# Kernel tuning notes

Hardware: AMD Instinct MI355X
Metric: run time of the kernel (lower is better)

Reference implementation:

```python
import jax, jax.numpy as jnp
import numpy as np

ARAP_WEIGHT = 1.0


def _decoder(code, W1, b1, W2, b2, W3, b3):
    # code: [D] -> vertices [N, 3]
    h = jax.nn.relu(code @ W1 + b1)
    h = jax.nn.relu(h @ W2 + b2)
    v = h @ W3 + b3
    return v.reshape(-1, 3)


def _arap_per_vertex(xyz1, recon, nbr, num_nbr, wmat):
    # xyz1, recon: [N,3]; nbr: [N,K] int; num_nbr: [N]; wmat: [N,K]
    N, K = nbr.shape
    mask = (jnp.arange(K)[None, :] < num_nbr[:, None]).astype(wmat.dtype)
    w = wmat * mask                              # zero out padded neighbors
    e_rest = xyz1[nbr] - xyz1[:, None, :]        # [N,K,3] rest-pose edges (gather)
    e_def = recon[nbr] - recon[:, None, :]       # [N,K,3] deformed edges (gather)
    # weighted covariance per vertex: S_i = sum_k w_ik e_ik e'_ik^T  -> [N,3,3]
    S = jnp.einsum('nk,nka,nkb->nab', w, e_rest, e_def)
    U, _, Vt = jnp.linalg.svd(S)
    V = jnp.swapaxes(Vt, -1, -2)
    R0 = jnp.einsum('nab,ncb->nac', V, U)        # V U^T
    d = jnp.linalg.det(R0)                       # reflection fix
    diag = jnp.stack([jnp.ones_like(d), jnp.ones_like(d), d], axis=-1)  # [N,3]
    R = jnp.einsum('nab,nb,ncb->nac', V, diag, U)
    R = jax.lax.stop_gradient(R)                 # local-global: rotations fixed in bwd
    e_rot = jnp.einsum('nab,nkb->nka', R, e_rest)
    resid = e_def - e_rot
    return jnp.sum(w * jnp.sum(resid * resid, axis=-1), axis=-1)  # [N]


def setup_inputs() -> dict:
    key = jax.random.key(0)
    ks = jax.random.split(key, 12)
    N, K, D = 20000, 16, 256
    H1, H2 = 512, 1024
    inp = {
        'code': jax.random.normal(ks[0], (D,), jnp.float32),
        'xyz1': jax.random.normal(ks[1], (N, 3), jnp.float32),
        'weightMatrix': jax.random.uniform(ks[2], (N, K), jnp.float32),
        'W1': jax.random.normal(ks[3], (D, H1), jnp.float32) * (1.0 / np.sqrt(D)),
        'b1': jax.random.normal(ks[4], (H1,), jnp.float32) * 0.01,
        'W2': jax.random.normal(ks[5], (H1, H2), jnp.float32) * (1.0 / np.sqrt(H1)),
        'b2': jax.random.normal(ks[6], (H2,), jnp.float32) * 0.01,
        'W3': jax.random.normal(ks[7], (H2, N * 3), jnp.float32) * (1.0 / np.sqrt(H2)),
        'b3': jax.random.normal(ks[8], (N * 3,), jnp.float32) * 0.01,
        'neighborsMatrix': jax.random.randint(ks[9], (N, K), 0, N, jnp.int64),
        'numNeighbors': jax.random.randint(ks[10], (N,), 0, 17, jnp.int64),
    }
    return inp


def reference(code, xyz1, weightMatrix, W1, b1, W2, b2, W3, b3,
              neighborsMatrix, numNeighbors):
    def energy(c):
        recon = _decoder(c, W1, b1, W2, b2, W3, b3)
        pv = _arap_per_vertex(xyz1, recon, neighborsMatrix, numNeighbors, weightMatrix)
        return ARAP_WEIGHT * jnp.mean(pv)

    E, g = jax.value_and_grad(energy)(code)
    # torch module returns (arapEnergy.item(), -code.grad) with arapEnergy = -E
    return (-E, g)
```

## Files before the change

### kernel.cpp

```cpp
#include <hip/hip_runtime.h>
#include <hip/hip_bf16.h>

#define N_V   20000
#define KNB   16
#define DCODE 256
#define H1    512
#define H2    1024
#define M3    60000

#define OFF_L2P   0
#define OFF_VPART 8192
#define OFF_V     488192
#define OFF_GV    548192
#define OFF_GZ2   608192
#define OFF_GZ1   609216
#define OFF_H1    609728
#define OFF_H2    610240
#define OFF_HC    611264
#define OFF_LIST  612288
#define OFF_CNT   613312
#define OFF_E     613316

__global__ void k_mlp12(const float* __restrict__ code, const float* __restrict__ W1,
                        const float* __restrict__ b1, const float* __restrict__ W2,
                        float* __restrict__ ws) {
    __shared__ float red[4][64];
    __shared__ float h1s[64];
    int t = threadIdx.x;
    int bx = blockIdx.x, dz = blockIdx.y;
    int d0 = dz * 64;

    int ln = t & 63, g = t >> 6;
    {
        float acc = 0.f;
        int r0 = g * 64;
#pragma unroll 8
        for (int rr = 0; rr < 64; ++rr)
            acc += code[r0 + rr] * W1[(size_t)(r0 + rr) * H1 + d0 + ln];
        red[g][ln] = acc;
    }
    __syncthreads();
    if (g == 0) {
        float h = fmaxf(red[0][ln] + red[1][ln] + red[2][ln] + red[3][ln] + b1[d0 + ln], 0.f);
        h1s[ln] = h;
        if (bx == 0) ws[OFF_H1 + d0 + ln] = h;
    }
    __syncthreads();

    int m = bx * 256 + t;
    float acc = 0.f;
#pragma unroll 8
    for (int dd = 0; dd < 64; ++dd)
        acc += h1s[dd] * W2[(size_t)(d0 + dd) * H2 + m];
    ws[OFF_L2P + dz * H2 + m] = acc;

    int gid = (dz * 4 + bx) * 256 + t;
    for (int idx = gid; idx < M3; idx += 8192) ws[OFF_GV + idx] = 0.f;
    if (gid == 0) { ws[OFF_E] = 0.f; ws[OFF_E + 1] = 0.f; }
}

__global__ void k_compact(const float* __restrict__ b2, float* __restrict__ ws) {
    __shared__ int scan[256];
    int t = threadIdx.x;
    float h[4]; int c = 0;
#pragma unroll
    for (int q = 0; q < 4; ++q) {
        int j = t * 4 + q;
        float s = b2[j];
#pragma unroll
        for (int p = 0; p < 8; ++p) s += ws[OFF_L2P + p * H2 + j];
        float hv = fmaxf(s, 0.f);
        ws[OFF_H2 + j] = hv;
        ws[OFF_GZ2 + j] = 0.f;
        h[q] = hv;
        c += (hv > 0.f) ? 1 : 0;
    }
    scan[t] = c;
    __syncthreads();
    for (int off = 1; off < 256; off <<= 1) {
        int x = (t >= off) ? scan[t - off] : 0;
        __syncthreads();
        scan[t] += x;
        __syncthreads();
    }
    int base = scan[t] - c;
    int* list = reinterpret_cast<int*>(&ws[OFF_LIST]);
#pragma unroll
    for (int q = 0; q < 4; ++q) {
        if (h[q] > 0.f) {
            list[base] = t * 4 + q;
            ws[OFF_HC + base] = h[q];
            ++base;
        }
    }
    if (t == 255) *reinterpret_cast<int*>(&ws[OFF_CNT]) = scan[255];
}

__global__ void k_l3p(const float* __restrict__ W3, float* __restrict__ ws) {
    __shared__ int   rlist[128];
    __shared__ float rh[128];
    int jz = blockIdx.y;
    int cnt = *reinterpret_cast<const int*>(&ws[OFF_CNT]);
    int per = (cnt + 7) >> 3;
    int s0 = jz * per;
    int s1 = s0 + per; if (s1 > cnt) s1 = cnt;
    int n = s1 - s0;
    int t = threadIdx.x;
    if (t < 128 && t < n) {
        rlist[t] = reinterpret_cast<const int*>(&ws[OFF_LIST])[s0 + t];
        rh[t]    = ws[OFF_HC + s0 + t];
    }
    __syncthreads();
    int m4 = blockIdx.x * 1024 + t * 4;
    if (m4 >= M3) return;
    float ax = 0.f, ay = 0.f, az = 0.f, aw = 0.f;
    int ii = 0;
    for (; ii + 7 < n; ii += 8) {
        float4 wv[8];
#pragma unroll
        for (int u = 0; u < 8; ++u)
            wv[u] = *reinterpret_cast<const float4*>(&W3[(size_t)rlist[ii + u] * M3 + m4]);
#pragma unroll
        for (int u = 0; u < 8; ++u) {
            float h = rh[ii + u];
            ax += h * wv[u].x; ay += h * wv[u].y; az += h * wv[u].z; aw += h * wv[u].w;
        }
    }
    for (; ii < n; ++ii) {
        float h = rh[ii];
        float4 wv = *reinterpret_cast<const float4*>(&W3[(size_t)rlist[ii] * M3 + m4]);
        ax += h * wv.x; ay += h * wv.y; az += h * wv.z; aw += h * wv.w;
    }
    *reinterpret_cast<float4*>(&ws[OFF_VPART + jz * M3 + m4]) =
        make_float4(ax, ay, az, aw);
}

__global__ void k_vred(const float* __restrict__ b3, float* __restrict__ ws) {
    int i4 = blockIdx.x * 256 + threadIdx.x;
    if (i4 < M3 / 4) {
        int m = i4 * 4;
        float4 a = *reinterpret_cast<const float4*>(&b3[m]);
#pragma unroll
        for (int jz = 0; jz < 8; ++jz) {
            float4 p = *reinterpret_cast<const float4*>(&ws[OFF_VPART + jz * M3 + m]);
            a.x += p.x; a.y += p.y; a.z += p.z; a.w += p.w;
        }
        *reinterpret_cast<float4*>(&ws[OFF_V + m]) = a;
    }
}


__device__ inline void jrotf(float a[3][3], float v[3][3], int p, int q) {
    float apq = a[p][q];
    if (fabsf(apq) < 1e-30f) return;
    float theta = (a[q][q] - a[p][p]) / (2.0f * apq);
    float t;
    if (fabsf(theta) > 1e18f) t = 0.5f / theta;
    else t = copysignf(1.0f, theta) / (fabsf(theta) + sqrtf(theta * theta + 1.0f));
    float c = 1.0f / sqrtf(t * t + 1.0f);
    float s = t * c;
    float app = a[p][p], aqq = a[q][q];
    a[p][p] = app - t * apq;
    a[q][q] = aqq + t * apq;
    a[p][q] = 0.0f; a[q][p] = 0.0f;
    int r = 3 - p - q;
    float arp = a[r][p], arq = a[r][q];
    a[r][p] = c * arp - s * arq; a[p][r] = a[r][p];
    a[r][q] = s * arp + c * arq; a[q][r] = a[r][q];
#pragma unroll
    for (int k2 = 0; k2 < 3; ++k2) {
        float vkp = v[k2][p], vkq = v[k2][q];
        v[k2][p] = c * vkp - s * vkq;
        v[k2][q] = s * vkp + c * vkq;
    }
}

__device__ void compute_Rf(const float S[3][3], float R[3][3]) {
    float A[3][3], V[3][3];
#pragma unroll
    for (int a = 0; a < 3; ++a)
#pragma unroll
        for (int b = 0; b < 3; ++b) {
            float s = 0.0f;
#pragma unroll
            for (int c = 0; c < 3; ++c) s += S[c][a] * S[c][b];
            A[a][b] = s;
            V[a][b] = (a == b) ? 1.0f : 0.0f;
        }
    for (int sweep = 0; sweep < 15; ++sweep) {
        float off = A[0][1]*A[0][1] + A[0][2]*A[0][2] + A[1][2]*A[1][2];
        float dg  = A[0][0]*A[0][0] + A[1][1]*A[1][1] + A[2][2]*A[2][2];
        if (off <= 1e-12f * (dg + 1e-30f)) break;
        jrotf(A, V, 0, 1); jrotf(A, V, 0, 2); jrotf(A, V, 1, 2);
    }
    int id[3] = {0, 1, 2};
    if (A[id[0]][id[0]] < A[id[1]][id[1]]) { int t = id[0]; id[0] = id[1]; id[1] = t; }
    if (A[id[0]][id[0]] < A[id[2]][id[2]]) { int t = id[0]; id[0] = id[2]; id[2] = t; }
    if (A[id[1]][id[1]] < A[id[2]][id[2]]) { int t = id[1]; id[1] = id[2]; id[2] = t; }
    float v0[3], v1[3], v2[3];
#pragma unroll
    for (int r = 0; r < 3; ++r) {
        v0[r] = V[r][id[0]]; v1[r] = V[r][id[1]]; v2[r] = V[r][id[2]];
    }
    float u0[3], u1[3], u2[3];
#pragma unroll
    for (int a = 0; a < 3; ++a)
        u0[a] = S[a][0]*v0[0] + S[a][1]*v0[1] + S[a][2]*v0[2];
    float n0 = sqrtf(u0[0]*u0[0] + u0[1]*u0[1] + u0[2]*u0[2]);
    if (!(n0 > 1e-20f)) {
#pragma unroll
        for (int a = 0; a < 3; ++a)
#pragma unroll
            for (int c = 0; c < 3; ++c) R[a][c] = (a == c) ? 1.0f : 0.0f;
        return;
    }
#pragma unroll
    for (int a = 0; a < 3; ++a) u0[a] /= n0;
    float t1[3];
#pragma unroll
    for (int a = 0; a < 3; ++a)
        t1[a] = S[a][0]*v1[0] + S[a][1]*v1[1] + S[a][2]*v1[2];
    float dp = u0[0]*t1[0] + u0[1]*t1[1] + u0[2]*t1[2];
#pragma unroll
    for (int a = 0; a < 3; ++a) t1[a] -= dp * u0[a];
    float n1 = sqrtf(t1[0]*t1[0] + t1[1]*t1[1] + t1[2]*t1[2]);
    if (n1 > 1e-5f * n0) {
#pragma unroll
        for (int a = 0; a < 3; ++a) u1[a] = t1[a] / n1;
    } else {
        int m = (fabsf(u0[0]) <= fabsf(u0[1]) && fabsf(u0[0]) <= fabsf(u0[2])) ? 0
              : (fabsf(u0[1]) <= fabsf(u0[2]) ? 1 : 2);
        float e[3] = {0.0f, 0.0f, 0.0f}; e[m] = 1.0f;
        float cx[3] = { u0[1]*e[2] - u0[2]*e[1],
                        u0[2]*e[0] - u0[0]*e[2],
                        u0[0]*e[1] - u0[1]*e[0] };
        float nn = sqrtf(cx[0]*cx[0] + cx[1]*cx[1] + cx[2]*cx[2]);
#pragma unroll
        for (int a = 0; a < 3; ++a) u1[a] = cx[a] / nn;
    }
    u2[0] = u0[1]*u1[2] - u0[2]*u1[1];
    u2[1] = u0[2]*u1[0] - u0[0]*u1[2];
    u2[2] = u0[0]*u1[1] - u0[1]*u1[0];
    float d = v0[0]*(v1[1]*v2[2] - v1[2]*v2[1])
            - v0[1]*(v1[0]*v2[2] - v1[2]*v2[0])
            + v0[2]*(v1[0]*v2[1] - v1[1]*v2[0]);
#pragma unroll
    for (int a = 0; a < 3; ++a)
#pragma unroll
        for (int c = 0; c < 3; ++c)
            R[a][c] = v0[a]*u0[c] + v1[a]*u1[c] + d * (v2[a]*u2[c]);
}

__global__ void k_arap(const float* __restrict__ xyz1, const float* __restrict__ wmat,
                       const int* __restrict__ nbr, const int* __restrict__ nnum,
                       float* __restrict__ ws) {
    const float* recon = ws + OFF_V;
    float* gv = ws + OFF_GV;
    int i = blockIdx.x * 256 + threadIdx.x;
    double pv = 0.0;
    if (i < N_V) {
        int num = nnum[i]; if (num > KNB) num = KNB;
        float cr0 = xyz1[3*i], cr1 = xyz1[3*i+1], cr2 = xyz1[3*i+2];
        float cd0 = recon[3*i], cd1 = recon[3*i+1], cd2 = recon[3*i+2];
        float er[KNB][3], ed[KNB][3], wk[KNB];
        int   jn[KNB];
        float S[3][3] = {{0,0,0},{0,0,0},{0,0,0}};
#pragma unroll
        for (int k = 0; k < KNB; ++k) {
            bool live = (k < num);
            int j = live ? nbr[i*KNB + k] : i;
            float w = live ? wmat[i*KNB + k] : 0.f;
            jn[k] = j; wk[k] = w;
            float e0 = xyz1[3*j]   - cr0, e1 = xyz1[3*j+1] - cr1, e2 = xyz1[3*j+2] - cr2;
            float f0 = recon[3*j]  - cd0, f1 = recon[3*j+1] - cd1, f2 = recon[3*j+2] - cd2;
            er[k][0] = e0; er[k][1] = e1; er[k][2] = e2;
            ed[k][0] = f0; ed[k][1] = f1; ed[k][2] = f2;
            S[0][0] += w*e0*f0; S[0][1] += w*e0*f1; S[0][2] += w*e0*f2;
            S[1][0] += w*e1*f0; S[1][1] += w*e1*f1; S[1][2] += w*e1*f2;
            S[2][0] += w*e2*f0; S[2][1] += w*e2*f1; S[2][2] += w*e2*f2;
        }
        float R[3][3];
        compute_Rf(S, R);
        const float gscale = 2.0f / (float)N_V;
        float own0 = 0.f, own1 = 0.f, own2 = 0.f;
#pragma unroll
        for (int k = 0; k < KNB; ++k) {
            if (k < num) {
                float w = wk[k];
                float r0 = ed[k][0] - (R[0][0]*er[k][0] + R[0][1]*er[k][1] + R[0][2]*er[k][2]);
                float r1 = ed[k][1] - (R[1][0]*er[k][0] + R[1][1]*er[k][1] + R[1][2]*er[k][2]);
                float r2 = ed[k][2] - (R[2][0]*er[k][0] + R[2][1]*er[k][1] + R[2][2]*er[k][2]);
                pv += (double)(w * (r0*r0 + r1*r1 + r2*r2));
                float g0 = gscale * w * r0;
                float g1 = gscale * w * r1;
                float g2 = gscale * w * r2;
                int j = jn[k];
                atomicAdd(&gv[3*j+0], g0);
                atomicAdd(&gv[3*j+1], g1);
                atomicAdd(&gv[3*j+2], g2);
                own0 += g0; own1 += g1; own2 += g2;
            }
        }
        if (num > 0) {
            atomicAdd(&gv[3*i+0], -own0);
            atomicAdd(&gv[3*i+1], -own1);
            atomicAdd(&gv[3*i+2], -own2);
        }
    }
#pragma unroll
    for (int m = 32; m; m >>= 1) pv += __shfl_xor(pv, m);
    __shared__ double wred[4];
    if ((threadIdx.x & 63) == 0) wred[threadIdx.x >> 6] = pv;
    __syncthreads();
    if (threadIdx.x == 0)
        atomicAdd(reinterpret_cast<double*>(ws + OFF_E),
                  wred[0] + wred[1] + wred[2] + wred[3]);
}


__global__ void k_gh2(const float* __restrict__ W3, float* __restrict__ ws) {
    int b = blockIdx.x;
    int cnt = *reinterpret_cast<const int*>(&ws[OFF_CNT]);
    if (2 * b >= cnt) return;
    const int* list = reinterpret_cast<const int*>(&ws[OFF_LIST]);
    int j0 = list[2 * b];
    bool has1 = (2 * b + 1 < cnt);
    int j1 = has1 ? list[2 * b + 1] : j0;
    const float4* w3r0 = reinterpret_cast<const float4*>(W3 + (size_t)j0 * M3);
    const float4* w3r1 = reinterpret_cast<const float4*>(W3 + (size_t)j1 * M3);
    const float4* gv4  = reinterpret_cast<const float4*>(ws + OFF_GV);
    float acc0 = 0.f, acc1 = 0.f;
    for (int it = threadIdx.x; it < M3 / 4; it += 256) {
        float4 g = gv4[it];
        float4 a = w3r0[it];
        float4 c = w3r1[it];
        acc0 += a.x*g.x + a.y*g.y + a.z*g.z + a.w*g.w;
        acc1 += c.x*g.x + c.y*g.y + c.z*g.z + c.w*g.w;
    }
    for (int m = 32; m; m >>= 1) {
        acc0 += __shfl_xor(acc0, m);
        acc1 += __shfl_xor(acc1, m);
    }
    __shared__ float wsum[4][2];
    if ((threadIdx.x & 63) == 0) {
        wsum[threadIdx.x >> 6][0] = acc0;
        wsum[threadIdx.x >> 6][1] = acc1;
    }
    __syncthreads();
    if (threadIdx.x == 0) {
        ws[OFF_GZ2 + j0] = wsum[0][0] + wsum[1][0] + wsum[2][0] + wsum[3][0];
        if (has1)
            ws[OFF_GZ2 + j1] = wsum[0][1] + wsum[1][1] + wsum[2][1] + wsum[3][1];
    }
}

__global__ void k_gh1(const float* __restrict__ W2, float* __restrict__ ws) {
    int wv = threadIdx.x >> 6, ln = threadIdx.x & 63;
    int i = blockIdx.x * 4 + wv;
    const float* gz2 = ws + OFF_GZ2;
    float acc = 0.f;
#pragma unroll
    for (int it = 0; it < H2 / 64; ++it) {
        int jj = ln + it * 64;
        acc += W2[(size_t)i * H2 + jj] * gz2[jj];
    }
    for (int m = 32; m; m >>= 1) acc += __shfl_xor(acc, m);
    if (ln == 0) ws[OFF_GZ1 + i] = (ws[OFF_H1 + i] > 0.f) ? acc : 0.f;
}

__global__ void k_gcode(const float* __restrict__ W1, float* __restrict__ ws,
                        float* __restrict__ out) {
    int wv = threadIdx.x >> 6, ln = threadIdx.x & 63;
    int d = blockIdx.x * 4 + wv;
    const float* gz1 = ws + OFF_GZ1;
    float acc = 0.f;
#pragma unroll
    for (int it = 0; it < H1 / 64; ++it) {
        int ii = ln + it * 64;
        acc += W1[(size_t)d * H1 + ii] * gz1[ii];
    }
    for (int m = 32; m; m >>= 1) acc += __shfl_xor(acc, m);
    if (ln == 0) out[1 + d] = acc;
    if (blockIdx.x == 0 && threadIdx.x == 0) {
        double E = *reinterpret_cast<const double*>(ws + OFF_E);
        out[0] = (float)(-(E / (double)N_V));
    }
}

extern "C" void kernel_launch(void* const* d_in, const int* in_sizes, int n_in,
                              void* d_out, int out_size, void* d_ws, size_t ws_size,
                              hipStream_t stream) {
    const float* code = (const float*)d_in[0];
    const float* xyz1 = (const float*)d_in[1];
    const float* wmat = (const float*)d_in[2];
    const float* W1   = (const float*)d_in[3];
    const float* b1   = (const float*)d_in[4];
    const float* W2   = (const float*)d_in[5];
    const float* b2   = (const float*)d_in[6];
    const float* W3   = (const float*)d_in[7];
    const float* b3   = (const float*)d_in[8];
    const int*   nbr  = (const int*)d_in[9];
    const int*   nnum = (const int*)d_in[10];
    float* out = (float*)d_out;
    float* ws  = (float*)d_ws;

    k_mlp12  <<<dim3(4, 8),  256, 0, stream>>>(code, W1, b1, W2, ws);
    k_compact<<<1,           256, 0, stream>>>(b2, ws);
    k_l3p    <<<dim3(59, 8), 256, 0, stream>>>(W3, ws);
    k_vred   <<<59,          256, 0, stream>>>(b3, ws);
    k_arap   <<<79,          256, 0, stream>>>(xyz1, wmat, nbr, nnum, ws);
    k_gh2    <<<512,         256, 0, stream>>>(W3, ws);
    k_gh1    <<<128,         256, 0, stream>>>(W2, ws);
    k_gcode  <<<64,          256, 0, stream>>>(W1, ws, out);
}
```

Measured before the change: 120.8 us.

## Fuse all stages into one cooperative persistent kernel with grid syncs

Replaces the eight-kernel launch sequence with a single cooperative kernel of 256 blocks that separates phases with grid.sync, removing per-launch overhead and the idle gaps between kernels. The layer-2 matvec is split across more blocks. The ARAP phase is remapped to one wave per 64 vertices, spread over the persistent grid, and re-gathers neighbours instead of holding them in register arrays. The Jacobi SVD now runs a fixed 6 sweeps with no convergence check and uses hardware rcp/rsq approximations. The fixed sweep count and fast reciprocals may cost accuracy, and each grid barrier has its own cost.

```diff
diff --git a/kernel.cpp b/kernel.cpp
--- a/kernel.cpp
+++ b/kernel.cpp
@@ -1,5 +1,8 @@
 #include <hip/hip_runtime.h>
+#include <hip/hip_cooperative_groups.h>
 #include <hip/hip_bf16.h>
+
+namespace cg = cooperative_groups;
 
 #define N_V   20000
 #define KNB   16
@@ -19,145 +22,18 @@
 #define OFF_HC    611264
 #define OFF_LIST  612288
 #define OFF_CNT   613312
-#define OFF_E     613316
-
-__global__ void k_mlp12(const float* __restrict__ code, const float* __restrict__ W1,
-                        const float* __restrict__ b1, const float* __restrict__ W2,
-                        float* __restrict__ ws) {
-    __shared__ float red[4][64];
-    __shared__ float h1s[64];
-    int t = threadIdx.x;
-    int bx = blockIdx.x, dz = blockIdx.y;
-    int d0 = dz * 64;
-
-    int ln = t & 63, g = t >> 6;
-    {
-        float acc = 0.f;
-        int r0 = g * 64;
-#pragma unroll 8
-        for (int rr = 0; rr < 64; ++rr)
-            acc += code[r0 + rr] * W1[(size_t)(r0 + rr) * H1 + d0 + ln];
-        red[g][ln] = acc;
-    }
-    __syncthreads();
-    if (g == 0) {
-        float h = fmaxf(red[0][ln] + red[1][ln] + red[2][ln] + red[3][ln] + b1[d0 + ln], 0.f);
-        h1s[ln] = h;
-        if (bx == 0) ws[OFF_H1 + d0 + ln] = h;
-    }
-    __syncthreads();
-
-    int m = bx * 256 + t;
-    float acc = 0.f;
-#pragma unroll 8
-    for (int dd = 0; dd < 64; ++dd)
-        acc += h1s[dd] * W2[(size_t)(d0 + dd) * H2 + m];
-    ws[OFF_L2P + dz * H2 + m] = acc;
-
-    int gid = (dz * 4 + bx) * 256 + t;
-    for (int idx = gid; idx < M3; idx += 8192) ws[OFF_GV + idx] = 0.f;
-    if (gid == 0) { ws[OFF_E] = 0.f; ws[OFF_E + 1] = 0.f; }
-}
-
-__global__ void k_compact(const float* __restrict__ b2, float* __restrict__ ws) {
-    __shared__ int scan[256];
-    int t = threadIdx.x;
-    float h[4]; int c = 0;
-#pragma unroll
-    for (int q = 0; q < 4; ++q) {
-        int j = t * 4 + q;
-        float s = b2[j];
-#pragma unroll
-        for (int p = 0; p < 8; ++p) s += ws[OFF_L2P + p * H2 + j];
-        float hv = fmaxf(s, 0.f);
-        ws[OFF_H2 + j] = hv;
-        ws[OFF_GZ2 + j] = 0.f;
-        h[q] = hv;
-        c += (hv > 0.f) ? 1 : 0;
-    }
-    scan[t] = c;
-    __syncthreads();
-    for (int off = 1; off < 256; off <<= 1) {
-        int x = (t >= off) ? scan[t - off] : 0;
-        __syncthreads();
-        scan[t] += x;
-        __syncthreads();
-    }
-    int base = scan[t] - c;
-    int* list = reinterpret_cast<int*>(&ws[OFF_LIST]);
-#pragma unroll
-    for (int q = 0; q < 4; ++q) {
-        if (h[q] > 0.f) {
-            list[base] = t * 4 + q;
-            ws[OFF_HC + base] = h[q];
-            ++base;
-        }
-    }
-    if (t == 255) *reinterpret_cast<int*>(&ws[OFF_CNT]) = scan[255];
-}
-
-__global__ void k_l3p(const float* __restrict__ W3, float* __restrict__ ws) {
-    __shared__ int   rlist[128];
-    __shared__ float rh[128];
-    int jz = blockIdx.y;
-    int cnt = *reinterpret_cast<const int*>(&ws[OFF_CNT]);
-    int per = (cnt + 7) >> 3;
-    int s0 = jz * per;
-    int s1 = s0 + per; if (s1 > cnt) s1 = cnt;
-    int n = s1 - s0;
-    int t = threadIdx.x;
-    if (t < 128 && t < n) {
-        rlist[t] = reinterpret_cast<const int*>(&ws[OFF_LIST])[s0 + t];
-        rh[t]    = ws[OFF_HC + s0 + t];
-    }
-    __syncthreads();
-    int m4 = blockIdx.x * 1024 + t * 4;
-    if (m4 >= M3) return;
-    float ax = 0.f, ay = 0.f, az = 0.f, aw = 0.f;
-    int ii = 0;
-    for (; ii + 7 < n; ii += 8) {
-        float4 wv[8];
-#pragma unroll
-        for (int u = 0; u < 8; ++u)
-            wv[u] = *reinterpret_cast<const float4*>(&W3[(size_t)rlist[ii + u] * M3 + m4]);
-#pragma unroll
-        for (int u = 0; u < 8; ++u) {
-            float h = rh[ii + u];
-            ax += h * wv[u].x; ay += h * wv[u].y; az += h * wv[u].z; aw += h * wv[u].w;
-        }
-    }
-    for (; ii < n; ++ii) {
-        float h = rh[ii];
-        float4 wv = *reinterpret_cast<const float4*>(&W3[(size_t)rlist[ii] * M3 + m4]);
-        ax += h * wv.x; ay += h * wv.y; az += h * wv.z; aw += h * wv.w;
-    }
-    *reinterpret_cast<float4*>(&ws[OFF_VPART + jz * M3 + m4]) =
-        make_float4(ax, ay, az, aw);
-}
-
-__global__ void k_vred(const float* __restrict__ b3, float* __restrict__ ws) {
-    int i4 = blockIdx.x * 256 + threadIdx.x;
-    if (i4 < M3 / 4) {
-        int m = i4 * 4;
-        float4 a = *reinterpret_cast<const float4*>(&b3[m]);
-#pragma unroll
-        for (int jz = 0; jz < 8; ++jz) {
-            float4 p = *reinterpret_cast<const float4*>(&ws[OFF_VPART + jz * M3 + m]);
-            a.x += p.x; a.y += p.y; a.z += p.z; a.w += p.w;
-        }
-        *reinterpret_cast<float4*>(&ws[OFF_V + m]) = a;
-    }
-}
-
+#define OFF_E     613314
+
+__device__ inline float frcp(float x) { return __builtin_amdgcn_rcpf(x); }
+__device__ inline float frsq(float x) { return __builtin_amdgcn_rsqf(x); }
 
 __device__ inline void jrotf(float a[3][3], float v[3][3], int p, int q) {
     float apq = a[p][q];
-    if (fabsf(apq) < 1e-30f) return;
-    float theta = (a[q][q] - a[p][p]) / (2.0f * apq);
-    float t;
-    if (fabsf(theta) > 1e18f) t = 0.5f / theta;
-    else t = copysignf(1.0f, theta) / (fabsf(theta) + sqrtf(theta * theta + 1.0f));
-    float c = 1.0f / sqrtf(t * t + 1.0f);
+    float den = 2.0f * apq;
+    float sden = copysignf(fmaxf(fabsf(den), 1e-30f), den);
+    float theta = (a[q][q] - a[p][p]) * frcp(sden);
+    float t = copysignf(1.0f, theta) * frcp(fabsf(theta) + sqrtf(theta * theta + 1.0f));
+    float c = frsq(t * t + 1.0f);
     float s = t * c;
     float app = a[p][p], aqq = a[q][q];
     a[p][p] = app - t * apq;
@@ -187,10 +63,7 @@
             A[a][b] = s;
             V[a][b] = (a == b) ? 1.0f : 0.0f;
         }
-    for (int sweep = 0; sweep < 15; ++sweep) {
-        float off = A[0][1]*A[0][1] + A[0][2]*A[0][2] + A[1][2]*A[1][2];
-        float dg  = A[0][0]*A[0][0] + A[1][1]*A[1][1] + A[2][2]*A[2][2];
-        if (off <= 1e-12f * (dg + 1e-30f)) break;
+    for (int sweep = 0; sweep < 6; ++sweep) {
         jrotf(A, V, 0, 1); jrotf(A, V, 0, 2); jrotf(A, V, 1, 2);
     }
     int id[3] = {0, 1, 2};
@@ -206,7 +79,8 @@
 #pragma unroll
     for (int a = 0; a < 3; ++a)
         u0[a] = S[a][0]*v0[0] + S[a][1]*v0[1] + S[a][2]*v0[2];
-    float n0 = sqrtf(u0[0]*u0[0] + u0[1]*u0[1] + u0[2]*u0[2]);
+    float nn0 = u0[0]*u0[0] + u0[1]*u0[1] + u0[2]*u0[2];
+    float n0 = sqrtf(nn0);
     if (!(n0 > 1e-20f)) {
 #pragma unroll
         for (int a = 0; a < 3; ++a)
@@ -214,8 +88,9 @@
             for (int c = 0; c < 3; ++c) R[a][c] = (a == c) ? 1.0f : 0.0f;
         return;
     }
-#pragma unroll
-    for (int a = 0; a < 3; ++a) u0[a] /= n0;
+    float rn0 = frcp(n0);
+#pragma unroll
+    for (int a = 0; a < 3; ++a) u0[a] *= rn0;
     float t1[3];
 #pragma unroll
     for (int a = 0; a < 3; ++a)
@@ -225,8 +100,9 @@
     for (int a = 0; a < 3; ++a) t1[a] -= dp * u0[a];
     float n1 = sqrtf(t1[0]*t1[0] + t1[1]*t1[1] + t1[2]*t1[2]);
     if (n1 > 1e-5f * n0) {
-#pragma unroll
-        for (int a = 0; a < 3; ++a) u1[a] = t1[a] / n1;
+        float rn1 = frcp(n1);
+#pragma unroll
+        for (int a = 0; a < 3; ++a) u1[a] = t1[a] * rn1;
     } else {
         int m = (fabsf(u0[0]) <= fabsf(u0[1]) && fabsf(u0[0]) <= fabsf(u0[2])) ? 0
               : (fabsf(u0[1]) <= fabsf(u0[2]) ? 1 : 2);
@@ -234,9 +110,9 @@
         float cx[3] = { u0[1]*e[2] - u0[2]*e[1],
                         u0[2]*e[0] - u0[0]*e[2],
                         u0[0]*e[1] - u0[1]*e[0] };
-        float nn = sqrtf(cx[0]*cx[0] + cx[1]*cx[1] + cx[2]*cx[2]);
-#pragma unroll
-        for (int a = 0; a < 3; ++a) u1[a] = cx[a] / nn;
+        float rnn = frsq(cx[0]*cx[0] + cx[1]*cx[1] + cx[2]*cx[2]);
+#pragma unroll
+        for (int a = 0; a < 3; ++a) u1[a] = cx[a] * rnn;
     }
     u2[0] = u0[1]*u1[2] - u0[2]*u1[1];
     u2[1] = u0[2]*u1[0] - u0[0]*u1[2];
@@ -251,139 +127,287 @@
             R[a][c] = v0[a]*u0[c] + v1[a]*u1[c] + d * (v2[a]*u2[c]);
 }
 
-__global__ void k_arap(const float* __restrict__ xyz1, const float* __restrict__ wmat,
-                       const int* __restrict__ nbr, const int* __restrict__ nnum,
-                       float* __restrict__ ws) {
-    const float* recon = ws + OFF_V;
-    float* gv = ws + OFF_GV;
-    int i = blockIdx.x * 256 + threadIdx.x;
-    double pv = 0.0;
-    if (i < N_V) {
-        int num = nnum[i]; if (num > KNB) num = KNB;
-        float cr0 = xyz1[3*i], cr1 = xyz1[3*i+1], cr2 = xyz1[3*i+2];
-        float cd0 = recon[3*i], cd1 = recon[3*i+1], cd2 = recon[3*i+2];
-        float er[KNB][3], ed[KNB][3], wk[KNB];
-        int   jn[KNB];
-        float S[3][3] = {{0,0,0},{0,0,0},{0,0,0}};
-#pragma unroll
-        for (int k = 0; k < KNB; ++k) {
-            bool live = (k < num);
-            int j = live ? nbr[i*KNB + k] : i;
-            float w = live ? wmat[i*KNB + k] : 0.f;
-            jn[k] = j; wk[k] = w;
-            float e0 = xyz1[3*j]   - cr0, e1 = xyz1[3*j+1] - cr1, e2 = xyz1[3*j+2] - cr2;
-            float f0 = recon[3*j]  - cd0, f1 = recon[3*j+1] - cd1, f2 = recon[3*j+2] - cd2;
-            er[k][0] = e0; er[k][1] = e1; er[k][2] = e2;
-            ed[k][0] = f0; ed[k][1] = f1; ed[k][2] = f2;
-            S[0][0] += w*e0*f0; S[0][1] += w*e0*f1; S[0][2] += w*e0*f2;
-            S[1][0] += w*e1*f0; S[1][1] += w*e1*f1; S[1][2] += w*e1*f2;
-            S[2][0] += w*e2*f0; S[2][1] += w*e2*f1; S[2][2] += w*e2*f2;
-        }
-        float R[3][3];
-        compute_Rf(S, R);
-        const float gscale = 2.0f / (float)N_V;
-        float own0 = 0.f, own1 = 0.f, own2 = 0.f;
-#pragma unroll
-        for (int k = 0; k < KNB; ++k) {
-            if (k < num) {
-                float w = wk[k];
-                float r0 = ed[k][0] - (R[0][0]*er[k][0] + R[0][1]*er[k][1] + R[0][2]*er[k][2]);
-                float r1 = ed[k][1] - (R[1][0]*er[k][0] + R[1][1]*er[k][1] + R[1][2]*er[k][2]);
-                float r2 = ed[k][2] - (R[2][0]*er[k][0] + R[2][1]*er[k][1] + R[2][2]*er[k][2]);
+__global__ __launch_bounds__(256, 1) void k_mega(
+    const float* __restrict__ code, const float* __restrict__ xyz1,
+    const float* __restrict__ wmat, const float* __restrict__ W1,
+    const float* __restrict__ b1,  const float* __restrict__ W2,
+    const float* __restrict__ b2,  const float* __restrict__ W3,
+    const float* __restrict__ b3,  const int* __restrict__ nbr,
+    const int* __restrict__ nnum,  float* __restrict__ out,
+    float* __restrict__ ws)
+{
+    cg::grid_group grid = cg::this_grid();
+    const int bid = blockIdx.x;
+    const int t = threadIdx.x;
+
+    __shared__ float red4[4][64];
+    __shared__ float h1s[64];
+    __shared__ float zp[8][32];
+    __shared__ int   scan[256];
+    __shared__ int   rlist[128];
+    __shared__ float rh[128];
+    __shared__ float wsum[4][2];
+
+    {
+        const int bx = bid & 31, dz = bid >> 5;
+        const int d0 = dz * 64;
+        const int ln = t & 63, g4 = t >> 6;
+        float acc = 0.f;
+        const int r0 = g4 * 64;
+#pragma unroll 8
+        for (int rr = 0; rr < 64; ++rr)
+            acc += code[r0 + rr] * W1[(size_t)(r0 + rr) * H1 + d0 + ln];
+        red4[g4][ln] = acc;
+        __syncthreads();
+        if (g4 == 0) {
+            float h = fmaxf(red4[0][ln] + red4[1][ln] + red4[2][ln] + red4[3][ln]
+                            + b1[d0 + ln], 0.f);
+            h1s[ln] = h;
+            if (bx == 0) ws[OFF_H1 + d0 + ln] = h;
+        }
+        __syncthreads();
+        const int col = t & 31, g8 = t >> 5;
+        const int m = bx * 32 + col;
+        float a2 = 0.f;
+        const int dd0 = g8 * 8;
+#pragma unroll
+        for (int dd = 0; dd < 8; ++dd)
+            a2 += h1s[dd0 + dd] * W2[(size_t)(d0 + dd0 + dd) * H2 + m];
+        zp[g8][col] = a2;
+        __syncthreads();
+        if (g8 == 0) {
+            float s = 0.f;
+#pragma unroll
+            for (int p = 0; p < 8; ++p) s += zp[p][col];
+            ws[OFF_L2P + dz * H2 + m] = s;
+        }
+        for (int idx = bid * 256 + t; idx < M3; idx += 65536)
+            ws[OFF_GV + idx] = 0.f;
+        if (bid == 0 && t == 0)
+            *reinterpret_cast<double*>(ws + OFF_E) = 0.0;
+    }
+    grid.sync();
+
+    if (bid == 0) {
+        float h[4]; int c = 0;
+#pragma unroll
+        for (int q = 0; q < 4; ++q) {
+            int j = t * 4 + q;
+            float s = b2[j];
+#pragma unroll
+            for (int p = 0; p < 8; ++p) s += ws[OFF_L2P + p * H2 + j];
+            float hv = fmaxf(s, 0.f);
+            ws[OFF_H2 + j] = hv;
+            ws[OFF_GZ2 + j] = 0.f;
+            h[q] = hv;
+            c += (hv > 0.f) ? 1 : 0;
+        }
+        scan[t] = c;
+        __syncthreads();
+        for (int off = 1; off < 256; off <<= 1) {
+            int x = (t >= off) ? scan[t - off] : 0;
+            __syncthreads();
+            scan[t] += x;
+            __syncthreads();
+        }
+        int base = scan[t] - c;
+        int* list = reinterpret_cast<int*>(&ws[OFF_LIST]);
+#pragma unroll
+        for (int q = 0; q < 4; ++q) {
+            if (h[q] > 0.f) {
+                list[base] = t * 4 + q;
+                ws[OFF_HC + base] = h[q];
+                ++base;
+            }
+        }
+        if (t == 255) *reinterpret_cast<int*>(&ws[OFF_CNT]) = scan[255];
+    }
+    grid.sync();
+
+    const int cnt = *reinterpret_cast<const int*>(&ws[OFF_CNT]);
+
+    {
+        const int jz = bid & 7;
+        const int bxA = bid >> 3;
+        const int per = (cnt + 7) >> 3;
+        int s0 = jz * per;
+        int s1 = s0 + per; if (s1 > cnt) s1 = cnt;
+        const int n = s1 - s0;
+        if (t < 128 && t < n) {
+            rlist[t] = reinterpret_cast<const int*>(&ws[OFF_LIST])[s0 + t];
+            rh[t]    = ws[OFF_HC + s0 + t];
+        }
+        __syncthreads();
+        for (int bx2 = bxA; bx2 < 59; bx2 += 32) {
+            int m4 = bx2 * 1024 + t * 4;
+            if (m4 < M3) {
+                float ax = 0.f, ay = 0.f, az = 0.f, aw = 0.f;
+                int ii = 0;
+                for (; ii + 7 < n; ii += 8) {
+                    float4 wv[8];
+#pragma unroll
+                    for (int u = 0; u < 8; ++u)
+                        wv[u] = *reinterpret_cast<const float4*>(
+                            &W3[(size_t)rlist[ii + u] * M3 + m4]);
+#pragma unroll
+                    for (int u = 0; u < 8; ++u) {
+                        float hq = rh[ii + u];
+                        ax += hq * wv[u].x; ay += hq * wv[u].y;
+                        az += hq * wv[u].z; aw += hq * wv[u].w;
+                    }
+                }
+                for (; ii < n; ++ii) {
+                    float hq = rh[ii];
+                    float4 wv = *reinterpret_cast<const float4*>(
+                        &W3[(size_t)rlist[ii] * M3 + m4]);
+                    ax += hq * wv.x; ay += hq * wv.y; az += hq * wv.z; aw += hq * wv.w;
+                }
+                *reinterpret_cast<float4*>(&ws[OFF_VPART + jz * M3 + m4]) =
+                    make_float4(ax, ay, az, aw);
+            }
+        }
+    }
+    grid.sync();
+
+    {
+        int i4 = bid * 256 + t;
+        if (i4 < M3 / 4) {
+            int m = i4 * 4;
+            float4 a = *reinterpret_cast<const float4*>(&b3[m]);
+#pragma unroll
+            for (int jz = 0; jz < 8; ++jz) {
+                float4 p = *reinterpret_cast<const float4*>(&ws[OFF_VPART + jz * M3 + m]);
+                a.x += p.x; a.y += p.y; a.z += p.z; a.w += p.w;
+            }
+            *reinterpret_cast<float4*>(&ws[OFF_V + m]) = a;
+        }
+    }
+    grid.sync();
+
+    {
+        const float* recon = ws + OFF_V;
+        float* gv = ws + OFF_GV;
+        const int wv = t >> 6, lane = t & 63;
+        const int gw = bid * 4 + wv;
+        int c = (gw * 313 + 1023) >> 10;
+        bool busy = (c < 313) && (((c << 10) / 313) == gw);
+        double pv = 0.0;
+        int i = c * 64 + lane;
+        if (busy && i < N_V) {
+            int num = nnum[i]; if (num > KNB) num = KNB;
+            float cr0 = xyz1[3*i], cr1 = xyz1[3*i+1], cr2 = xyz1[3*i+2];
+            float cd0 = recon[3*i], cd1 = recon[3*i+1], cd2 = recon[3*i+2];
+            float S[3][3] = {{0,0,0},{0,0,0},{0,0,0}};
+            for (int k = 0; k < num; ++k) {
+                int j = nbr[i*KNB + k];
+                float w = wmat[i*KNB + k];
+                float e0 = xyz1[3*j]  - cr0, e1 = xyz1[3*j+1] - cr1, e2 = xyz1[3*j+2] - cr2;
+                float f0 = recon[3*j] - cd0, f1 = recon[3*j+1] - cd1, f2 = recon[3*j+2] - cd2;
+                S[0][0] += w*e0*f0; S[0][1] += w*e0*f1; S[0][2] += w*e0*f2;
+                S[1][0] += w*e1*f0; S[1][1] += w*e1*f1; S[1][2] += w*e1*f2;
+                S[2][0] += w*e2*f0; S[2][1] += w*e2*f1; S[2][2] += w*e2*f2;
+            }
+            float R[3][3];
+            compute_Rf(S, R);
+            const float gscale = 2.0f / (float)N_V;
+            float own0 = 0.f, own1 = 0.f, own2 = 0.f;
+            for (int k = 0; k < num; ++k) {
+                int j = nbr[i*KNB + k];
+                float w = wmat[i*KNB + k];
+                float e0 = xyz1[3*j]  - cr0, e1 = xyz1[3*j+1] - cr1, e2 = xyz1[3*j+2] - cr2;
+                float f0 = recon[3*j] - cd0, f1 = recon[3*j+1] - cd1, f2 = recon[3*j+2] - cd2;
+                float r0 = f0 - (R[0][0]*e0 + R[0][1]*e1 + R[0][2]*e2);
+                float r1 = f1 - (R[1][0]*e0 + R[1][1]*e1 + R[1][2]*e2);
+                float r2 = f2 - (R[2][0]*e0 + R[2][1]*e1 + R[2][2]*e2);
                 pv += (double)(w * (r0*r0 + r1*r1 + r2*r2));
                 float g0 = gscale * w * r0;
                 float g1 = gscale * w * r1;
                 float g2 = gscale * w * r2;
-                int j = jn[k];
                 atomicAdd(&gv[3*j+0], g0);
                 atomicAdd(&gv[3*j+1], g1);
                 atomicAdd(&gv[3*j+2], g2);
                 own0 += g0; own1 += g1; own2 += g2;
             }
-        }
-        if (num > 0) {
-            atomicAdd(&gv[3*i+0], -own0);
-            atomicAdd(&gv[3*i+1], -own1);
-            atomicAdd(&gv[3*i+2], -own2);
-        }
-    }
-#pragma unroll
-    for (int m = 32; m; m >>= 1) pv += __shfl_xor(pv, m);
-    __shared__ double wred[4];
-    if ((threadIdx.x & 63) == 0) wred[threadIdx.x >> 6] = pv;
-    __syncthreads();
-    if (threadIdx.x == 0)
-        atomicAdd(reinterpret_cast<double*>(ws + OFF_E),
-                  wred[0] + wred[1] + wred[2] + wred[3]);
-}
-
-
-__global__ void k_gh2(const float* __restrict__ W3, float* __restrict__ ws) {
-    int b = blockIdx.x;
-    int cnt = *reinterpret_cast<const int*>(&ws[OFF_CNT]);
-    if (2 * b >= cnt) return;
-    const int* list = reinterpret_cast<const int*>(&ws[OFF_LIST]);
-    int j0 = list[2 * b];
-    bool has1 = (2 * b + 1 < cnt);
-    int j1 = has1 ? list[2 * b + 1] : j0;
-    const float4* w3r0 = reinterpret_cast<const float4*>(W3 + (size_t)j0 * M3);
-    const float4* w3r1 = reinterpret_cast<const float4*>(W3 + (size_t)j1 * M3);
-    const float4* gv4  = reinterpret_cast<const float4*>(ws + OFF_GV);
-    float acc0 = 0.f, acc1 = 0.f;
-    for (int it = threadIdx.x; it < M3 / 4; it += 256) {
-        float4 g = gv4[it];
-        float4 a = w3r0[it];
-        float4 c = w3r1[it];
-        acc0 += a.x*g.x + a.y*g.y + a.z*g.z + a.w*g.w;
-        acc1 += c.x*g.x + c.y*g.y + c.z*g.z + c.w*g.w;
-    }
-    for (int m = 32; m; m >>= 1) {
-        acc0 += __shfl_xor(acc0, m);
-        acc1 += __shfl_xor(acc1, m);
-    }
-    __shared__ float wsum[4][2];
-    if ((threadIdx.x & 63) == 0) {
-        wsum[threadIdx.x >> 6][0] = acc0;
-        wsum[threadIdx.x >> 6][1] = acc1;
-    }
-    __syncthreads();
-    if (threadIdx.x == 0) {
-        ws[OFF_GZ2 + j0] = wsum[0][0] + wsum[1][0] + wsum[2][0] + wsum[3][0];
-        if (has1)
-            ws[OFF_GZ2 + j1] = wsum[0][1] + wsum[1][1] + wsum[2][1] + wsum[3][1];
-    }
-}
-
-__global__ void k_gh1(const float* __restrict__ W2, float* __restrict__ ws) {
-    int wv = threadIdx.x >> 6, ln = threadIdx.x & 63;
-    int i = blockIdx.x * 4 + wv;
-    const float* gz2 = ws + OFF_GZ2;
-    float acc = 0.f;
-#pragma unroll
-    for (int it = 0; it < H2 / 64; ++it) {
-        int jj = ln + it * 64;
-        acc += W2[(size_t)i * H2 + jj] * gz2[jj];
-    }
-    for (int m = 32; m; m >>= 1) acc += __shfl_xor(acc, m);
-    if (ln == 0) ws[OFF_GZ1 + i] = (ws[OFF_H1 + i] > 0.f) ? acc : 0.f;
-}
-
-__global__ void k_gcode(const float* __restrict__ W1, float* __restrict__ ws,
-                        float* __restrict__ out) {
-    int wv = threadIdx.x >> 6, ln = threadIdx.x & 63;
-    int d = blockIdx.x * 4 + wv;
-    const float* gz1 = ws + OFF_GZ1;
-    float acc = 0.f;
-#pragma unroll
-    for (int it = 0; it < H1 / 64; ++it) {
-        int ii = ln + it * 64;
-        acc += W1[(size_t)d * H1 + ii] * gz1[ii];
-    }
-    for (int m = 32; m; m >>= 1) acc += __shfl_xor(acc, m);
-    if (ln == 0) out[1 + d] = acc;
-    if (blockIdx.x == 0 && threadIdx.x == 0) {
-        double E = *reinterpret_cast<const double*>(ws + OFF_E);
-        out[0] = (float)(-(E / (double)N_V));
+            if (num > 0) {
+                atomicAdd(&gv[3*i+0], -own0);
+                atomicAdd(&gv[3*i+1], -own1);
+                atomicAdd(&gv[3*i+2], -own2);
+            }
+        }
+#pragma unroll
+        for (int m = 32; m; m >>= 1) pv += __shfl_xor(pv, m);
+        if (busy && lane == 0)
+            atomicAdd(reinterpret_cast<double*>(ws + OFF_E), pv);
+    }
+    grid.sync();
+
+    {
+        int b = bid;
+        if (2 * b < cnt) {
+            const int* list = reinterpret_cast<const int*>(&ws[OFF_LIST]);
+            int j0 = list[2 * b];
+            bool has1 = (2 * b + 1 < cnt);
+            int j1 = has1 ? list[2 * b + 1] : j0;
+            const float4* w3r0 = reinterpret_cast<const float4*>(W3 + (size_t)j0 * M3);
+            const float4* w3r1 = reinterpret_cast<const float4*>(W3 + (size_t)j1 * M3);
+            const float4* gv4  = reinterpret_cast<const float4*>(ws + OFF_GV);
+            float acc0 = 0.f, acc1 = 0.f;
+            for (int it = t; it < M3 / 4; it += 256) {
+                float4 g = gv4[it];
+                float4 a = w3r0[it];
+                float4 cc = w3r1[it];
+                acc0 += a.x*g.x + a.y*g.y + a.z*g.z + a.w*g.w;
+                acc1 += cc.x*g.x + cc.y*g.y + cc.z*g.z + cc.w*g.w;
+            }
+            for (int m = 32; m; m >>= 1) {
+                acc0 += __shfl_xor(acc0, m);
+                acc1 += __shfl_xor(acc1, m);
+            }
+            if ((t & 63) == 0) {
+                wsum[t >> 6][0] = acc0;
+                wsum[t >> 6][1] = acc1;
+            }
+            __syncthreads();
+            if (t == 0) {
+                ws[OFF_GZ2 + j0] = wsum[0][0] + wsum[1][0] + wsum[2][0] + wsum[3][0];
+                if (has1)
+                    ws[OFF_GZ2 + j1] = wsum[0][1] + wsum[1][1] + wsum[2][1] + wsum[3][1];
+            }
+        }
+    }
+    grid.sync();
+
+    {
+        const int wv = t >> 6, ln = t & 63;
+        const int gw = bid * 4 + wv;
+        if (gw < H1) {
+            const float* gz2 = ws + OFF_GZ2;
+            float acc = 0.f;
+#pragma unroll
+            for (int it = 0; it < H2 / 64; ++it)
+                acc += W2[(size_t)gw * H2 + ln + it * 64] * gz2[ln + it * 64];
+            for (int m = 32; m; m >>= 1) acc += __shfl_xor(acc, m);
+            if (ln == 0) ws[OFF_GZ1 + gw] = (ws[OFF_H1 + gw] > 0.f) ? acc : 0.f;
+        }
+    }
+    grid.sync();
+
+    {
+        const int wv = t >> 6, ln = t & 63;
+        const int gw = bid * 4 + wv;
+        if (gw < DCODE) {
+            const float* gz1 = ws + OFF_GZ1;
+            float acc = 0.f;
+#pragma unroll
+            for (int it = 0; it < H1 / 64; ++it)
+                acc += W1[(size_t)gw * H1 + ln + it * 64] * gz1[ln + it * 64];
+            for (int m = 32; m; m >>= 1) acc += __shfl_xor(acc, m);
+            if (ln == 0) out[1 + gw] = acc;
+        }
+        if (bid == 0 && t == 0) {
+            double E = *reinterpret_cast<const double*>(ws + OFF_E);
+            out[0] = (float)(-(E / (double)N_V));
+        }
     }
 }
 
@@ -404,12 +428,10 @@
     float* out = (float*)d_out;
     float* ws  = (float*)d_ws;
 
-    k_mlp12  <<<dim3(4, 8),  256, 0, stream>>>(code, W1, b1, W2, ws);
-    k_compact<<<1,           256, 0, stream>>>(b2, ws);
-    k_l3p    <<<dim3(59, 8), 256, 0, stream>>>(W3, ws);
-    k_vred   <<<59,          256, 0, stream>>>(b3, ws);
-    k_arap   <<<79,          256, 0, stream>>>(xyz1, wmat, nbr, nnum, ws);
-    k_gh2    <<<512,         256, 0, stream>>>(W3, ws);
-    k_gh1    <<<128,         256, 0, stream>>>(W2, ws);
-    k_gcode  <<<64,          256, 0, stream>>>(W1, ws, out);
+    void* args[] = { (void*)&code, (void*)&xyz1, (void*)&wmat, (void*)&W1,
+                     (void*)&b1,   (void*)&W2,   (void*)&b2,   (void*)&W3,
+                     (void*)&b3,   (void*)&nbr,  (void*)&nnum, (void*)&out,
+                     (void*)&ws };
+    hipLaunchCooperativeKernel((const void*)k_mega, dim3(256), dim3(256),
+                               args, 0, stream);
 }
```

Result: slower. 305.6 us (+153.0%).
